# Optimization experiments

Measured on AMD Instinct MI355X. Metric: run time of the kernel, lower is better.

Reference implementation:

```python
import jax, jax.numpy as jnp
import numpy as np

V, D, H, L, F, S, B = 32000, 1024, 16, 4, 4096, 1024, 2
THETA = 10000.0
EPS = 1e-5


def rmsnorm(x, w):
    # faithful to source: rms = sqrt(mean(x^2)) + eps (eps OUTSIDE the sqrt)
    rms = jnp.sqrt(jnp.mean(x * x, axis=-1, keepdims=True)) + EPS
    return (x / rms) * w


def rope(x, pos):
    # x: [B, H, S, dk]; rotate interleaved even/odd pairs
    dk = x.shape[-1]
    inv_freq = 1.0 / (THETA ** (jnp.arange(0, dk, 2, dtype=jnp.float32) / dk))
    ang = pos[:, None].astype(jnp.float32) * inv_freq[None, :]  # [S, dk/2]
    cos, sin = jnp.cos(ang), jnp.sin(ang)
    x1, x2 = x[..., ::2], x[..., 1::2]
    r1 = x1 * cos - x2 * sin
    r2 = x1 * sin + x2 * cos
    return jnp.stack([r1, r2], axis=-1).reshape(x.shape)


def setup_inputs() -> dict:
    key = jax.random.key(0)
    ks = jax.random.split(key, 12)
    s_attn = np.sqrt(2.0 / (D + D)).astype(np.float32)
    s_ffn = np.sqrt(2.0 / (F + D)).astype(np.float32)
    s_head = np.sqrt(2.0 / (V + D)).astype(np.float32)
    return {
        "token_ids": jax.random.randint(ks[0], (B, S), 0, V),
        "tok_emb": jax.random.normal(ks[1], (V, D), jnp.float32),
        "lm_head_w": jax.random.normal(ks[2], (V, D), jnp.float32) * s_head,
        "ln_final_w": jnp.ones((D,), jnp.float32),
        "q_w": jax.random.normal(ks[3], (L, D, D), jnp.float32) * s_attn,
        "k_w": jax.random.normal(ks[4], (L, D, D), jnp.float32) * s_attn,
        "v_w": jax.random.normal(ks[5], (L, D, D), jnp.float32) * s_attn,
        "o_w": jax.random.normal(ks[6], (L, D, D), jnp.float32) * s_attn,
        "ln1_w": jnp.ones((L, D), jnp.float32),
        "ln2_w": jnp.ones((L, D), jnp.float32),
        "w1": jax.random.normal(ks[7], (L, F, D), jnp.float32) * s_ffn,
        "w2": jax.random.normal(ks[8], (L, D, F), jnp.float32) * s_ffn,
        "w3": jax.random.normal(ks[9], (L, F, D), jnp.float32) * s_ffn,
    }


def reference(token_ids, tok_emb, lm_head_w, ln_final_w, q_w, k_w, v_w, o_w,
              ln1_w, ln2_w, w1, w2, w3):
    b, s = token_ids.shape
    dk = D // H
    scale = 1.0 / np.sqrt(dk).astype(np.float32)
    pos = jnp.arange(s)
    causal = jnp.tril(jnp.ones((s, s), dtype=bool))  # mask[i,j] = i >= j
    x = tok_emb[token_ids]  # [B, S, D]

    for l in range(L):
        # attention block with RoPE
        h = rmsnorm(x, ln1_w[l])
        q = (h @ q_w[l].T).reshape(b, s, H, dk).transpose(0, 2, 1, 3)
        k = (h @ k_w[l].T).reshape(b, s, H, dk).transpose(0, 2, 1, 3)
        v = (h @ v_w[l].T).reshape(b, s, H, dk).transpose(0, 2, 1, 3)
        q = rope(q, pos)
        k = rope(k, pos)
        scores = jnp.einsum('bhqd,bhkd->bhqk', q, k) * scale
        scores = jnp.where(causal, scores, -jnp.inf)
        attn = jax.nn.softmax(scores, axis=-1)
        o = jnp.einsum('bhqk,bhkd->bhqd', attn, v)
        o = o.transpose(0, 2, 1, 3).reshape(b, s, D)
        x = x + o @ o_w[l].T

        # SwiGLU FFN block
        h2 = rmsnorm(x, ln2_w[l])
        xw = h2 @ w1[l].T                       # [B, S, F]
        swish = xw * jax.nn.sigmoid(xw)
        x = x + (swish * (h2 @ w3[l].T)) @ w2[l].T

    x = rmsnorm(x, ln_final_w)
    return x @ lm_head_w.T  # logits [B, S, V]
```

## Files before the change

### kernel.cpp

```cpp
#include <hip/hip_runtime.h>
#include <math.h>

#define V_SZ 32000
#define D_SZ 1024
#define H_SZ 16
#define L_SZ 4
#define F_SZ 4096
#define S_SZ 1024
#define B_SZ 2
#define DK 64
#define NTOK (B_SZ * S_SZ)
#define NEG_INF -3.0e38f

typedef _Float16 half8 __attribute__((ext_vector_type(8)));
typedef _Float16 half4 __attribute__((ext_vector_type(4)));
typedef float floatx4 __attribute__((ext_vector_type(4)));

__device__ __forceinline__ void gload16(const void* g, void* l) {
    __builtin_amdgcn_global_load_lds(
        (const __attribute__((address_space(1))) unsigned int*)g,
        (__attribute__((address_space(3))) unsigned int*)l, 16, 0, 0);
}

__global__ __launch_bounds__(256) void f2h4(const float* __restrict__ s0,
                                            const float* __restrict__ s1,
                                            const float* __restrict__ s2,
                                            const float* __restrict__ s3,
                                            _Float16* __restrict__ d, int n8each) {
    const int i = blockIdx.x * 256 + threadIdx.x;
    const int sel = i / n8each;
    const int off = i - sel * n8each;
    const float* s = sel == 0 ? s0 : (sel == 1 ? s1 : (sel == 2 ? s2 : s3));
    const float4 a = ((const float4*)s)[2 * off];
    const float4 b = ((const float4*)s)[2 * off + 1];
    half8 h = {(_Float16)a.x, (_Float16)a.y, (_Float16)a.z, (_Float16)a.w,
               (_Float16)b.x, (_Float16)b.y, (_Float16)b.z, (_Float16)b.w};
    ((half8*)d)[i] = h;
}

__global__ __launch_bounds__(256) void f2h3(const float* __restrict__ s0,
                                            const float* __restrict__ s1,
                                            const float* __restrict__ s2,
                                            _Float16* __restrict__ d, int n8each) {
    const int i = blockIdx.x * 256 + threadIdx.x;
    const int sel = i / n8each;
    const int off = i - sel * n8each;
    const float* s = sel == 0 ? s0 : (sel == 1 ? s1 : s2);
    const float4 a = ((const float4*)s)[2 * off];
    const float4 b = ((const float4*)s)[2 * off + 1];
    half8 h = {(_Float16)a.x, (_Float16)a.y, (_Float16)a.z, (_Float16)a.w,
               (_Float16)b.x, (_Float16)b.y, (_Float16)b.z, (_Float16)b.w};
    ((half8*)d)[i] = h;
}

__global__ __launch_bounds__(256) void f2h(const float* __restrict__ in,
                                           _Float16* __restrict__ out, int n8) {
    const int i = blockIdx.x * 256 + threadIdx.x;
    if (i >= n8) return;
    const float4 a = ((const float4*)in)[2 * i];
    const float4 b = ((const float4*)in)[2 * i + 1];
    half8 h = {(_Float16)a.x, (_Float16)a.y, (_Float16)a.z, (_Float16)a.w,
               (_Float16)b.x, (_Float16)b.y, (_Float16)b.z, (_Float16)b.w};
    ((half8*)out)[i] = h;
}

__global__ __launch_bounds__(256) void embed_kernel(const int* __restrict__ ids,
                                                    const float* __restrict__ emb,
                                                    float* __restrict__ x) {
    const int row = blockIdx.x;
    const int id = ids[row];
    const float4* src = (const float4*)(emb + (size_t)id * D_SZ);
    float4* dst = (float4*)(x + (size_t)row * D_SZ);
    dst[threadIdx.x] = src[threadIdx.x];
}

__global__ __launch_bounds__(256) void rmsnorm_kernel(const float* __restrict__ x,
                                                      const float* __restrict__ w,
                                                      _Float16* __restrict__ out) {
    const int row = blockIdx.x;
    const int tid = threadIdx.x;
    const float4 v = ((const float4*)(x + (size_t)row * D_SZ))[tid];
    float ss = v.x * v.x + v.y * v.y + v.z * v.z + v.w * v.w;
#pragma unroll
    for (int off = 32; off > 0; off >>= 1) ss += __shfl_down(ss, off, 64);
    __shared__ float red[4];
    if ((tid & 63) == 0) red[tid >> 6] = ss;
    __syncthreads();
    const float tot = red[0] + red[1] + red[2] + red[3];
    const float inv = 1.0f / (sqrtf(tot * (1.0f / (float)D_SZ)) + 1e-5f);
    const float4 wv = ((const float4*)w)[tid];
    half4 o = {(_Float16)(v.x * inv * wv.x), (_Float16)(v.y * inv * wv.y),
               (_Float16)(v.z * inv * wv.z), (_Float16)(v.w * inv * wv.w)};
    ((half4*)(out + (size_t)row * D_SZ))[tid] = o;
}

template <int EPI, bool MFAST, int TM>
__global__ __launch_bounds__(256) void hgemm(const _Float16* __restrict__ A,
                                             const _Float16* __restrict__ B,
                                             float* __restrict__ Cf,
                                             _Float16* Ch,
                                             const _Float16* AUXh,
                                             _Float16* Cq,
                                             _Float16* Ck,
                                             _Float16* Cv,
                                             int M, int N, int K) {
    constexpr int WN = (TM == 128) ? 2 : 4;
    constexpr int CW = 128 / WN;
    constexpr int FN = CW / 16;
    __shared__ __align__(16) _Float16 As[2][TM * 32];
    __shared__ __align__(16) _Float16 Bs[2][128 * 32];
    const int tid = threadIdx.x;
    const int lane = tid & 63;
    const int wave = tid >> 6;
    const int wr = (TM == 128) ? (wave >> 1) : 0;
    const int wc = (TM == 128) ? (wave & 1) : wave;
    const int l15 = lane & 15, g = lane >> 4;

    const int gm = M / TM, gn = N >> 7, nwg = gm * gn;
    const int orig = blockIdx.x;
    const int q8 = nwg >> 3, r8 = nwg & 7, xcd = orig & 7, j8 = orig >> 3;
    const int wgid = (xcd < r8 ? xcd * (q8 + 1) : r8 * (q8 + 1) + (xcd - r8) * q8) + j8;
    const int bm = MFAST ? (wgid % gm) : (wgid / gn);
    const int bn = MFAST ? (wgid / gm) : (wgid % gn);
    const int m0 = bm * TM, n0 = bn * 128;

    const int offA0 = wave * (TM * 16) + lane * 16;
    const int offA1 = offA0 + 1024;
    const int rA0 = offA0 >> 6, kA0 = offA0 & 63;
    const int rA1 = offA1 >> 6, kA1 = offA1 & 63;
    const int offB0 = wave * 2048 + lane * 16;
    const int offB1 = offB0 + 1024;
    const int rB0 = offB0 >> 6, kB0 = offB0 & 63;
    const int rB1 = offB1 >> 6, kB1 = offB1 & 63;
    const char* gA0 = (const char*)(A + (size_t)(m0 + rA0) * K) + kA0;
    const char* gA1 = (const char*)(A + (size_t)(m0 + rA1) * K) + kA1;
    const char* gB0 = (const char*)(B + (size_t)(n0 + rB0) * K) + kB0;
    const char* gB1 = (const char*)(B + (size_t)(n0 + rB1) * K) + kB1;

#define STAGE(buf)                                                     \
    do {                                                               \
        gload16(gA0, (char*)As[buf] + offA0);                          \
        if constexpr (TM == 128) gload16(gA1, (char*)As[buf] + offA1); \
        gload16(gB0, (char*)Bs[buf] + offB0);                          \
        gload16(gB1, (char*)Bs[buf] + offB1);                          \
        gA0 += 64; gA1 += 64; gB0 += 64; gB1 += 64;                    \
    } while (0)

    floatx4 acc[4][FN];
#pragma unroll
    for (int i = 0; i < 4; i++)
#pragma unroll
        for (int j = 0; j < FN; j++) acc[i][j] = 0;

    STAGE(0);
    __syncthreads();
    int cur = 0;
    for (int kk = 0; kk < K; kk += 32) {
        if (kk + 32 < K) STAGE(cur ^ 1);
        half8 aF[4], bF[FN];
#pragma unroll
        for (int i = 0; i < 4; i++)
            aF[i] = *(const half8*)&As[cur][(wr * 64 + i * 16 + l15) * 32 + g * 8];
#pragma unroll
        for (int j = 0; j < FN; j++)
            bF[j] = *(const half8*)&Bs[cur][(wc * CW + j * 16 + l15) * 32 + g * 8];
#pragma unroll
        for (int i = 0; i < 4; i++)
#pragma unroll
            for (int j = 0; j < FN; j++)
                acc[i][j] = __builtin_amdgcn_mfma_f32_16x16x32_f16(aF[i], bF[j], acc[i][j], 0, 0, 0);
        __syncthreads();
        cur ^= 1;
    }
#undef STAGE

    const int rb = m0 + wr * 64 + g * 4;
    const int cb = n0 + wc * CW + l15;
    if (EPI == 4) {
        const int sel = n0 >> 10;
        _Float16* Cx = sel == 0 ? Cq : (sel == 1 ? Ck : Cv);
        const int cb0 = cb - sel * 1024;
#pragma unroll
        for (int i = 0; i < 4; i++) {
#pragma unroll
            for (int e = 0; e < 4; e++) {
                const int row = rb + i * 16 + e;
                const int pos = row & (S_SZ - 1);
#pragma unroll
                for (int j = 0; j < FN; j++) {
                    float v = acc[i][j][e];
                    const int col = cb0 + j * 16;
                    if (sel < 2) {
                        const float p = __shfl_xor(v, 1, 64);
                        const int pi = (col & 63) >> 1;
                        const float invf = exp2f((float)pi * -0.41524101186f);
                        float sn, cs;
                        sincosf((float)pos * invf, &sn, &cs);
                        v = (col & 1) ? (p * sn + v * cs) : (v * cs - p * sn);
                    }
                    Cx[(size_t)row * 1024 + col] = (_Float16)v;
                }
            }
        }
        return;
    }
#pragma unroll
    for (int i = 0; i < 4; i++) {
#pragma unroll
        for (int e = 0; e < 4; e++) {
            const int row = rb + i * 16 + e;
#pragma unroll
            for (int j = 0; j < FN; j++) {
                const float v = acc[i][j][e];
                if (EPI == 0) {
                    Cf[(size_t)row * N + cb + j * 16] = v;
                } else if (EPI == 1) {
                    Cf[(size_t)row * N + cb + j * 16] += v;
                } else if (EPI == 2) {
                    Ch[(size_t)row * N + cb + j * 16] =
                        (_Float16)(v / (1.0f + __expf(-v)));
                } else if (EPI == 3) {
                    const size_t idx = (size_t)row * N + cb + j * 16;
                    Ch[idx] = (_Float16)((float)AUXh[idx] * v);
                }
            }
        }
    }
}

__global__ __launch_bounds__(256) void vtrans(const _Float16* __restrict__ vh,
                                              _Float16* __restrict__ vt) {
    __shared__ __align__(16) _Float16 Ls[64][80];
    const int t = threadIdx.x;
    const int s0 = blockIdx.x * 64;
    const int bh = blockIdx.y;
    const int b = bh >> 4, h = bh & 15;
#pragma unroll
    for (int p = 0; p < 2; ++p) {
        const int sl = p * 32 + (t >> 3);
        const int d = (t & 7) * 8;
        *(half8*)&Ls[sl][d] =
            *(const half8*)&vh[((size_t)b * S_SZ + s0 + sl) * D_SZ + h * 64 + d];
    }
    __syncthreads();
#pragma unroll
    for (int p = 0; p < 2; ++p) {
        const int d = p * 32 + (t >> 3);
        const int sc = (t & 7) * 8;
        half8 v;
#pragma unroll
        for (int j = 0; j < 8; ++j) v[j] = Ls[sc + j][d];
        *(half8*)&vt[((size_t)bh * 64 + d) * S_SZ + s0 + sc] = v;
    }
}

__global__ __launch_bounds__(256) void attn_mfma(const _Float16* __restrict__ qh,
                                                 const _Float16* __restrict__ kh,
                                                 const _Float16* __restrict__ vt,
                                                 _Float16* __restrict__ o) {
    __shared__ __align__(16) _Float16 Ks[2][64 * 64];
    __shared__ __align__(16) _Float16 Vs[2][64 * 64];
    __shared__ __align__(16) _Float16 Ps[4][16][88];
    const int tid = threadIdx.x;
    const int lane = tid & 63, wave = tid >> 6;
    const int l15 = lane & 15, g = lane >> 4;
    const int bx = blockIdx.x;
    const int bh = blockIdx.y;
    const int h = bh & 15;
    const size_t tokb = (size_t)(bh >> 4) * S_SZ;

    const int qt0 = bx, qt1 = 15 - bx;
    const int qb0 = qt0 * 64, qb1 = qt1 * 64;
    const int ktmax = qt1;

    const int qrow = l15 * 4 + wave;
    half8 qA0[2], qA1[2];
#pragma unroll
    for (int kk = 0; kk < 2; ++kk) {
        qA0[kk] = *(const half8*)&qh[(tokb + qb0 + qrow) * D_SZ + h * 64 + kk * 32 + g * 8];
        qA1[kk] = *(const half8*)&qh[(tokb + qb1 + qrow) * D_SZ + h * 64 + kk * 32 + g * 8];
    }

    floatx4 accO0[4], accO1[4];
#pragma unroll
    for (int s = 0; s < 4; s++) { accO0[s] = 0; accO1[s] = 0; }
    float m0_[4] = {NEG_INF, NEG_INF, NEG_INF, NEG_INF};
    float l0_[4] = {0.0f, 0.0f, 0.0f, 0.0f};
    float m1_[4] = {NEG_INF, NEG_INF, NEG_INF, NEG_INF};
    float l1_[4] = {0.0f, 0.0f, 0.0f, 0.0f};

    const char* KbB = (const char*)(kh + tokb * D_SZ + h * 64);
    const char* VbB = (const char*)(vt + (size_t)bh * 64 * S_SZ);
    const int so0 = wave * 2048 + lane * 16;
    const int so1 = so0 + 1024;
    const int r0 = so0 >> 7, c0 = (so0 >> 4) & 7;
    const int r1 = so1 >> 7, c1 = (so1 >> 4) & 7;
    const int gc0 = ((c0 ^ (r0 & 7)) << 4);
    const int gc1 = ((c1 ^ (r1 & 7)) << 4);

#define STAGEKV(buf, kt)                                                   \
    do {                                                                   \
        const size_t kvr = (size_t)(kt) * 64;                              \
        gload16(KbB + (kvr + r0) * 2048 + gc0, (char*)Ks[buf] + so0);      \
        gload16(KbB + (kvr + r1) * 2048 + gc1, (char*)Ks[buf] + so1);      \
        gload16(VbB + r0 * 2048 + kvr * 2 + gc0, (char*)Vs[buf] + so0);    \
        gload16(VbB + r1 * 2048 + kvr * 2 + gc1, (char*)Vs[buf] + so1);    \
    } while (0)

#define LDSW(arr, rr, cc) \
    (*(const half8*)&(arr)[(rr) * 64 + ((((cc) ^ ((rr) & 7))) << 3)])

    auto computeTile = [&](const half8* qA, floatx4* accO, float* m_, float* l_,
                           int qbase, int kt, bool diag, int buf) {
        const int kv0 = kt * 64;
        floatx4 accS[4];
#pragma unroll
        for (int sub = 0; sub < 4; ++sub) {
            accS[sub] = 0;
#pragma unroll
            for (int kk = 0; kk < 2; ++kk) {
                half8 kB = LDSW(Ks[buf], sub * 16 + l15, kk * 4 + g);
                accS[sub] = __builtin_amdgcn_mfma_f32_16x16x32_f16(qA[kk], kB, accS[sub], 0, 0, 0);
            }
        }
        float sv[4][4];
        float mx[4] = {NEG_INF, NEG_INF, NEG_INF, NEG_INF};
#pragma unroll
        for (int sub = 0; sub < 4; ++sub)
#pragma unroll
            for (int e = 0; e < 4; ++e) {
                float s = accS[sub][e] * 0.125f;
                if (diag && (kv0 + sub * 16 + l15 > qbase + (g * 4 + e) * 4 + wave))
                    s = NEG_INF;
                sv[sub][e] = s;
                mx[e] = fmaxf(mx[e], s);
            }
#pragma unroll
        for (int msk = 1; msk <= 8; msk <<= 1)
#pragma unroll
            for (int e = 0; e < 4; ++e)
                mx[e] = fmaxf(mx[e], __shfl_xor(mx[e], msk, 64));
        float sf[4];
#pragma unroll
        for (int e = 0; e < 4; ++e) {
            const float mn = fmaxf(m_[e], mx[e]);
            sf[e] = __expf(m_[e] - mn);
            m_[e] = mn;
        }
        float rs[4] = {0.0f, 0.0f, 0.0f, 0.0f};
#pragma unroll
        for (int sub = 0; sub < 4; ++sub)
#pragma unroll
            for (int e = 0; e < 4; ++e) {
                const float p = __expf(sv[sub][e] - m_[e]);
                sv[sub][e] = p;
                rs[e] += p;
            }
#pragma unroll
        for (int msk = 1; msk <= 8; msk <<= 1)
#pragma unroll
            for (int e = 0; e < 4; ++e)
                rs[e] += __shfl_xor(rs[e], msk, 64);
#pragma unroll
        for (int e = 0; e < 4; ++e) l_[e] = l_[e] * sf[e] + rs[e];
#pragma unroll
        for (int sub = 0; sub < 4; ++sub)
#pragma unroll
            for (int e = 0; e < 4; ++e) accO[sub][e] *= sf[e];
#pragma unroll
        for (int sub = 0; sub < 4; ++sub)
#pragma unroll
            for (int e = 0; e < 4; ++e)
                Ps[wave][g * 4 + e][sub * 16 + l15] = (_Float16)sv[sub][e];
        half8 aP[2];
        aP[0] = *(const half8*)&Ps[wave][l15][g * 8];
        aP[1] = *(const half8*)&Ps[wave][l15][32 + g * 8];
#pragma unroll
        for (int sub = 0; sub < 4; ++sub)
#pragma unroll
            for (int kk = 0; kk < 2; ++kk) {
                half8 vB = LDSW(Vs[buf], sub * 16 + l15, kk * 4 + g);
                accO[sub] = __builtin_amdgcn_mfma_f32_16x16x32_f16(aP[kk], vB, accO[sub], 0, 0, 0);
            }
    };

    STAGEKV(0, 0);
    __syncthreads();
    int cur = 0;
    for (int kt = 0; kt <= ktmax; ++kt) {
        if (kt < ktmax) STAGEKV(cur ^ 1, kt + 1);
        computeTile(qA1, accO1, m1_, l1_, qb1, kt, kt == qt1, cur);
        if (kt <= qt0)
            computeTile(qA0, accO0, m0_, l0_, qb0, kt, kt == qt0, cur);
        __syncthreads();
        cur ^= 1;
    }
#undef STAGEKV
#undef LDSW

#pragma unroll
    for (int sub = 0; sub < 4; ++sub)
#pragma unroll
        for (int e = 0; e < 4; ++e) {
            const int rr = (g * 4 + e) * 4 + wave;
            o[(tokb + qb1 + rr) * D_SZ + h * 64 + sub * 16 + l15] =
                (_Float16)(accO1[sub][e] / l1_[e]);
            o[(tokb + qb0 + rr) * D_SZ + h * 64 + sub * 16 + l15] =
                (_Float16)(accO0[sub][e] / l0_[e]);
        }
}

extern "C" void kernel_launch(void* const* d_in, const int* in_sizes, int n_in,
                              void* d_out, int out_size, void* d_ws, size_t ws_size,
                              hipStream_t stream) {
    const int*   token_ids  = (const int*)d_in[0];
    const float* tok_emb    = (const float*)d_in[1];
    const float* lm_head_w  = (const float*)d_in[2];
    const float* ln_final_w = (const float*)d_in[3];
    const float* q_w        = (const float*)d_in[4];
    const float* k_w        = (const float*)d_in[5];
    const float* v_w        = (const float*)d_in[6];
    const float* o_w        = (const float*)d_in[7];
    const float* ln1_w      = (const float*)d_in[8];
    const float* ln2_w      = (const float*)d_in[9];
    const float* w1         = (const float*)d_in[10];
    const float* w2         = (const float*)d_in[11];
    const float* w3         = (const float*)d_in[12];
    float* out = (float*)d_out;

    char* W = (char*)d_ws;
    const size_t MB = 1u << 20;
    float*    x    = (float*)(W + 0);
    _Float16* h    = (_Float16*)(W + 8 * MB);
    _Float16* ao   = (_Float16*)(W + 12 * MB);
    _Float16* wq   = (_Float16*)(W + 16 * MB);
    _Float16* wo   = wq + 3 * (1u << 20);
    _Float16* ww1  = (_Float16*)(W + 24 * MB);
    _Float16* ww3  = ww1 + (F_SZ * D_SZ);
    _Float16* ww2  = ww3 + (F_SZ * D_SZ);
    _Float16* qh   = (_Float16*)(W + 48 * MB);
    _Float16* kh   = (_Float16*)(W + 52 * MB);
    _Float16* vh   = (_Float16*)(W + 56 * MB);
    _Float16* vt   = (_Float16*)(W + 60 * MB);
    _Float16* ff1h = (_Float16*)(W + 64 * MB);
    _Float16* whead = (_Float16*)(W + 24 * MB);

    embed_kernel<<<NTOK, 256, 0, stream>>>(token_ids, tok_emb, x);

    const int nDD8 = D_SZ * D_SZ / 8;
    const int nFD8 = F_SZ * D_SZ / 8;
    const dim3 gQKV(3 * D_SZ / 128 * (NTOK / 128));
    const dim3 gD64(D_SZ / 128 * (NTOK / 64));
    const dim3 gF(F_SZ / 128 * (NTOK / 128));
    const dim3 gATT(S_SZ / 128, B_SZ * H_SZ);
    const dim3 gVT(S_SZ / 64, B_SZ * H_SZ);

    for (int l = 0; l < L_SZ; l++) {
        const size_t oDD = (size_t)l * D_SZ * D_SZ;
        const size_t oFD = (size_t)l * F_SZ * D_SZ;
        rmsnorm_kernel<<<NTOK, 256, 0, stream>>>(x, ln1_w + (size_t)l * D_SZ, h);
        f2h4<<<4 * nDD8 / 256, 256, 0, stream>>>(q_w + oDD, k_w + oDD, v_w + oDD,
                                                 o_w + oDD, wq, nDD8);
        f2h3<<<3 * nFD8 / 256, 256, 0, stream>>>(w1 + oFD, w3 + oFD, w2 + oFD,
                                                 ww1, nFD8);
        hgemm<4, true, 128><<<gQKV, 256, 0, stream>>>(h, wq, nullptr, nullptr, nullptr,
                                                      qh, kh, vh, NTOK, 3 * D_SZ, D_SZ);
        vtrans<<<gVT, 256, 0, stream>>>(vh, vt);
        attn_mfma<<<gATT, 256, 0, stream>>>(qh, kh, vt, ao);
        hgemm<1, false, 64><<<gD64, 256, 0, stream>>>(ao, wo, x, nullptr, nullptr,
                                                      nullptr, nullptr, nullptr, NTOK, D_SZ, D_SZ);
        rmsnorm_kernel<<<NTOK, 256, 0, stream>>>(x, ln2_w + (size_t)l * D_SZ, h);
        hgemm<2, true, 128><<<gF, 256, 0, stream>>>(h, ww1, nullptr, ff1h, nullptr,
                                                    nullptr, nullptr, nullptr, NTOK, F_SZ, D_SZ);
        hgemm<3, true, 128><<<gF, 256, 0, stream>>>(h, ww3, nullptr, ff1h, ff1h,
                                                    nullptr, nullptr, nullptr, NTOK, F_SZ, D_SZ);
        hgemm<1, false, 64><<<gD64, 256, 0, stream>>>(ff1h, ww2, x, nullptr, nullptr,
                                                      nullptr, nullptr, nullptr, NTOK, D_SZ, F_SZ);
    }
    rmsnorm_kernel<<<NTOK, 256, 0, stream>>>(x, ln_final_w, h);
    const int nVD8 = V_SZ * D_SZ / 8;
    f2h<<<(nVD8 + 255) / 256, 256, 0, stream>>>(lm_head_w, whead, nVD8);
    const dim3 gOUT(V_SZ / 128 * (NTOK / 128));
    hgemm<0, true, 128><<<gOUT, 256, 0, stream>>>(h, whead, out, nullptr, nullptr,
                                                  nullptr, nullptr, nullptr, NTOK, V_SZ, D_SZ);
}
```

Before: 1.286 ms.

## Add 256x256 4-stage GEMM kernel; fuse w1/w3 into one GEMM and use for LM head

Adds a new 512-thread GEMM kernel with 256x256 tiles, a 4-deep LDS ring filled by direct global-to-LDS loads, XCD-aware block remapping and swizzled LDS reads. The w1 and w3 projections now run as one GEMM over concatenated weights: the first half gets the SiLU epilogue and the second half is stored raw, then a separate elementwise kernel multiplies them. The LM head also moves to the large-tile kernel. The aim is more data reuse per tile and fewer launches for the FFN up-projection, at the cost of one extra elementwise pass and heavier register and LDS use per block.

Result: faster. 1.261 ms (-2.0%).

```diff
diff --git a/kernel.cpp b/kernel.cpp
--- a/kernel.cpp
+++ b/kernel.cpp
@@ -64,6 +64,17 @@
     ((half8*)out)[i] = h;
 }
 
+__global__ __launch_bounds__(256) void hmul(_Float16* __restrict__ a,
+                                            const _Float16* __restrict__ b, int n8) {
+    const int i = blockIdx.x * 256 + threadIdx.x;
+    if (i >= n8) return;
+    half8 x = ((half8*)a)[i];
+    const half8 y = ((const half8*)b)[i];
+#pragma unroll
+    for (int j = 0; j < 8; ++j) x[j] = (_Float16)((float)x[j] * (float)y[j]);
+    ((half8*)a)[i] = x;
+}
+
 __global__ __launch_bounds__(256) void embed_kernel(const int* __restrict__ ids,
                                                     const float* __restrict__ emb,
                                                     float* __restrict__ x) {
@@ -92,6 +103,109 @@
     half4 o = {(_Float16)(v.x * inv * wv.x), (_Float16)(v.y * inv * wv.y),
                (_Float16)(v.z * inv * wv.z), (_Float16)(v.w * inv * wv.w)};
     ((half4*)(out + (size_t)row * D_SZ))[tid] = o;
+}
+
+template <int EPI8, bool MFAST>
+__global__ __launch_bounds__(512, 2) void hgemm8(const _Float16* __restrict__ A,
+                                                 const _Float16* __restrict__ B,
+                                                 float* __restrict__ Cf,
+                                                 _Float16* __restrict__ Ch1,
+                                                 _Float16* __restrict__ Ch3,
+                                                 int M, int N, int K) {
+    __shared__ __align__(16) _Float16 As[4][256 * 32];
+    __shared__ __align__(16) _Float16 Bs[4][256 * 32];
+    const int tid = threadIdx.x;
+    const int lane = tid & 63, wave = tid >> 6;
+    const int wm = wave >> 2, wn = wave & 3;
+    const int l15 = lane & 15, g = lane >> 4;
+
+    const int gm = M >> 8, gn = N >> 8, nwg = gm * gn;
+    const int orig = blockIdx.x;
+    const int q8 = nwg >> 3, r8 = nwg & 7, xcd = orig & 7, j8 = orig >> 3;
+    const int wgid = (xcd < r8 ? xcd * (q8 + 1) : r8 * (q8 + 1) + (xcd - r8) * q8) + j8;
+    const int bm = MFAST ? (wgid % gm) : (wgid / gn);
+    const int bn = MFAST ? (wgid / gm) : (wgid % gn);
+    const int m0 = bm << 8, n0 = bn << 8;
+
+    const int row0 = tid >> 2, row1 = 128 + (tid >> 2);
+    const int p = tid & 3;
+    const int c0 = p ^ ((row0 >> 1) & 3);
+    const int c1 = p ^ ((row1 >> 1) & 3);
+    const char* gA0 = (const char*)A + (size_t)(m0 + row0) * 2 * K + c0 * 16;
+    const char* gA1 = (const char*)A + (size_t)(m0 + row1) * 2 * K + c1 * 16;
+    const char* gB0 = (const char*)B + (size_t)(n0 + row0) * 2 * K + c0 * 16;
+    const char* gB1 = (const char*)B + (size_t)(n0 + row1) * 2 * K + c1 * 16;
+    const int loff0 = tid * 16, loff1 = 8192 + tid * 16;
+
+#define STAGE8(t)                                          \
+    do {                                                   \
+        const int _b = (t) & 3;                            \
+        const size_t _o = (size_t)(t) * 64;                \
+        gload16(gA0 + _o, (char*)As[_b] + loff0);          \
+        gload16(gA1 + _o, (char*)As[_b] + loff1);          \
+        gload16(gB0 + _o, (char*)Bs[_b] + loff0);          \
+        gload16(gB1 + _o, (char*)Bs[_b] + loff1);          \
+    } while (0)
+
+    floatx4 acc[8][4];
+#pragma unroll
+    for (int i = 0; i < 8; i++)
+#pragma unroll
+        for (int j = 0; j < 4; j++) acc[i][j] = 0;
+
+    const int nt = K >> 5;
+    STAGE8(0);
+    STAGE8(1);
+    STAGE8(2);
+    for (int t = 0; t < nt; ++t) {
+        const int rem = nt - 1 - t;
+        if (rem >= 2)      asm volatile("s_waitcnt vmcnt(8)" ::: "memory");
+        else if (rem == 1) asm volatile("s_waitcnt vmcnt(4)" ::: "memory");
+        else               asm volatile("s_waitcnt vmcnt(0)" ::: "memory");
+        __builtin_amdgcn_s_barrier();
+        __builtin_amdgcn_sched_barrier(0);
+        if (t + 3 < nt) STAGE8(t + 3);
+        const int buf = t & 3;
+        half8 bF[4], aF[8];
+#pragma unroll
+        for (int j = 0; j < 4; j++) {
+            const int R = wn * 64 + j * 16 + l15;
+            bF[j] = *(const half8*)&Bs[buf][R * 32 + (g ^ ((R >> 1) & 3)) * 8];
+        }
+#pragma unroll
+        for (int i = 0; i < 8; i++) {
+            const int R = wm * 128 + i * 16 + l15;
+            aF[i] = *(const half8*)&As[buf][R * 32 + (g ^ ((R >> 1) & 3)) * 8];
+        }
+#pragma unroll
+        for (int i = 0; i < 8; i++)
+#pragma unroll
+            for (int j = 0; j < 4; j++)
+                acc[i][j] = __builtin_amdgcn_mfma_f32_16x16x32_f16(aF[i], bF[j], acc[i][j], 0, 0, 0);
+    }
+#undef STAGE8
+
+#pragma unroll
+    for (int i = 0; i < 8; i++) {
+#pragma unroll
+        for (int e = 0; e < 4; e++) {
+            const int row = m0 + wm * 128 + i * 16 + g * 4 + e;
+#pragma unroll
+            for (int j = 0; j < 4; j++) {
+                const int col = n0 + wn * 64 + j * 16 + l15;
+                const float v = acc[i][j][e];
+                if (EPI8 == 0) {
+                    Cf[(size_t)row * N + col] = v;
+                } else {
+                    if (col < 4096)
+                        Ch1[(size_t)row * 4096 + col] =
+                            (_Float16)(v / (1.0f + __expf(-v)));
+                    else
+                        Ch3[(size_t)row * 4096 + col - 4096] = (_Float16)v;
+                }
+            }
+        }
+    }
 }
 
 template <int EPI, bool MFAST, int TM>
@@ -191,12 +305,12 @@
                     float v = acc[i][j][e];
                     const int col = cb0 + j * 16;
                     if (sel < 2) {
-                        const float p = __shfl_xor(v, 1, 64);
+                        const float pp = __shfl_xor(v, 1, 64);
                         const int pi = (col & 63) >> 1;
                         const float invf = exp2f((float)pi * -0.41524101186f);
                         float sn, cs;
                         sincosf((float)pos * invf, &sn, &cs);
-                        v = (col & 1) ? (p * sn + v * cs) : (v * cs - p * sn);
+                        v = (col & 1) ? (pp * sn + v * cs) : (v * cs - pp * sn);
                     }
                     Cx[(size_t)row * 1024 + col] = (_Float16)v;
                 }
@@ -436,12 +550,12 @@
     _Float16* wq   = (_Float16*)(W + 16 * MB);
     _Float16* wo   = wq + 3 * (1u << 20);
     _Float16* ww1  = (_Float16*)(W + 24 * MB);
-    _Float16* ww3  = ww1 + (F_SZ * D_SZ);
-    _Float16* ww2  = ww3 + (F_SZ * D_SZ);
+    _Float16* ww2  = ww1 + 2 * (F_SZ * D_SZ);
     _Float16* qh   = (_Float16*)(W + 48 * MB);
     _Float16* kh   = (_Float16*)(W + 52 * MB);
     _Float16* vh   = (_Float16*)(W + 56 * MB);
     _Float16* vt   = (_Float16*)(W + 60 * MB);
+    _Float16* ff3h = (_Float16*)(W + 48 * MB);
     _Float16* ff1h = (_Float16*)(W + 64 * MB);
     _Float16* whead = (_Float16*)(W + 24 * MB);
 
@@ -451,7 +565,7 @@
     const int nFD8 = F_SZ * D_SZ / 8;
     const dim3 gQKV(3 * D_SZ / 128 * (NTOK / 128));
     const dim3 gD64(D_SZ / 128 * (NTOK / 64));
-    const dim3 gF(F_SZ / 128 * (NTOK / 128));
+    const dim3 gW13(2 * F_SZ / 256 * (NTOK / 256));
     const dim3 gATT(S_SZ / 128, B_SZ * H_SZ);
     const dim3 gVT(S_SZ / 64, B_SZ * H_SZ);
 
@@ -470,17 +584,16 @@
         hgemm<1, false, 64><<<gD64, 256, 0, stream>>>(ao, wo, x, nullptr, nullptr,
                                                       nullptr, nullptr, nullptr, NTOK, D_SZ, D_SZ);
         rmsnorm_kernel<<<NTOK, 256, 0, stream>>>(x, ln2_w + (size_t)l * D_SZ, h);
-        hgemm<2, true, 128><<<gF, 256, 0, stream>>>(h, ww1, nullptr, ff1h, nullptr,
-                                                    nullptr, nullptr, nullptr, NTOK, F_SZ, D_SZ);
-        hgemm<3, true, 128><<<gF, 256, 0, stream>>>(h, ww3, nullptr, ff1h, ff1h,
-                                                    nullptr, nullptr, nullptr, NTOK, F_SZ, D_SZ);
+        hgemm8<1, true><<<gW13, 512, 0, stream>>>(h, ww1, nullptr, ff1h, ff3h,
+                                                  NTOK, 2 * F_SZ, D_SZ);
+        hmul<<<NTOK * F_SZ / 8 / 256, 256, 0, stream>>>(ff1h, ff3h, NTOK * F_SZ / 8);
         hgemm<1, false, 64><<<gD64, 256, 0, stream>>>(ff1h, ww2, x, nullptr, nullptr,
                                                       nullptr, nullptr, nullptr, NTOK, D_SZ, F_SZ);
     }
     rmsnorm_kernel<<<NTOK, 256, 0, stream>>>(x, ln_final_w, h);
     const int nVD8 = V_SZ * D_SZ / 8;
     f2h<<<(nVD8 + 255) / 256, 256, 0, stream>>>(lm_head_w, whead, nVD8);
-    const dim3 gOUT(V_SZ / 128 * (NTOK / 128));
-    hgemm<0, true, 128><<<gOUT, 256, 0, stream>>>(h, whead, out, nullptr, nullptr,
-                                                  nullptr, nullptr, nullptr, NTOK, V_SZ, D_SZ);
-}
+    const dim3 gOUT(V_SZ / 256 * (NTOK / 256));
+    hgemm8<0, true><<<gOUT, 512, 0, stream>>>(h, whead, out, nullptr, nullptr,
+                                              NTOK, V_SZ, D_SZ);
+}
```
